# Kernel tuning notes

Hardware: AMD Instinct MI355X
Metric: run time of the kernel (lower is better)

Reference implementation:

```python
import jax, jax.numpy as jnp
import numpy as np

NUM_SYMBOLS = 5
NUM_SUBCARRIERS = 33


def _dft_matrix(n):
    # Unitary DFT matrix: F[j,k] = exp(-2i*pi*j*k/n) / sqrt(n)
    omega = np.exp(-2j * np.pi / n)
    j, k = np.meshgrid(np.arange(n), np.arange(n))
    return (np.power(omega, j * k) / np.sqrt(n)).astype(np.complex64)


def setup_inputs() -> dict:
    key = jax.random.key(0)
    k1, k2 = jax.random.split(key)
    shape = (4096, NUM_SYMBOLS, 4, 4, NUM_SUBCARRIERS)  # (N, S, TXH, TXW, W)
    x_real = jax.random.normal(k1, shape, dtype=jnp.float32)
    x_imag = jax.random.normal(k2, shape, dtype=jnp.float32)
    F_sym = _dft_matrix(NUM_SYMBOLS)
    F_sub = _dft_matrix(NUM_SUBCARRIERS)
    return {
        "x_real": x_real,
        "x_imag": x_imag,
        "F_sym_real": jnp.asarray(F_sym.real, dtype=jnp.float32),
        "F_sym_imag": jnp.asarray(F_sym.imag, dtype=jnp.float32),
        "F_sub_real": jnp.asarray(F_sub.real, dtype=jnp.float32),
        "F_sub_imag": jnp.asarray(F_sub.imag, dtype=jnp.float32),
    }


def reference(x_real, x_imag, F_sym_real, F_sym_imag, F_sub_real, F_sub_imag):
    N, S, TXH, TXW, W = x_real.shape
    x = jax.lax.complex(x_real, x_imag).reshape(N, S, TXH * TXW, W)
    x = jnp.transpose(x, (0, 2, 1, 3))  # (N, A, S, W), A = TXH*TXW

    F_sym = jax.lax.complex(F_sym_real, F_sym_imag)  # (S, S)
    F_sub = jax.lax.complex(F_sub_real, F_sub_imag)  # (W, W)

    # 2D DFT across symbols (left) and subcarriers (right)
    X = jnp.einsum("st,natw->nasw", F_sym, x)
    X = jnp.einsum("nasw,wv->nasv", X, F_sub)

    # magnitude-square (power spectrum)
    X_mag_sq = (X.real * X.real + X.imag * X.imag).astype(jnp.complex64)

    # inverse 2D DFT (conjugate transposes) -> autocorrelation
    X = jnp.einsum("st,natw->nasw", F_sym.conj().T, X_mag_sq)
    X = jnp.einsum("nasw,wv->nasv", X, F_sub.conj().T)

    X = jnp.transpose(X, (0, 2, 1, 3))  # (N, S, A, W)
    return X.reshape(N, S, TXH, TXW, W)
```

## Files before the change

### kernel.cpp

```cpp
#include <hip/hip_runtime.h>

#define NS 5
#define NW 33
#define NA 16
#define SW 165
#define BUFS 99
#define MPW 5
#define GM 20
#define TPM 11
#define CPT 3
#define THREADS 256

#define C0T 3
#define C0E (C0T*NW*MPW)
#define IT0 8
#define C1T 2
#define C1E (C1T*NW*MPW)
#define IT1 6

typedef float f2 __attribute__((ext_vector_type(2)));

__device__ __forceinline__ void cmac_re(f2& z, f2 u, f2 f) {
    asm("v_pk_fma_f32 %0, %1, %2, %0 op_sel:[0,0,0] op_sel_hi:[1,0,1]"
        : "+v"(z) : "v"(u), "v"(f));
}
__device__ __forceinline__ void cmac_im(f2& z, f2 d, f2 f) {
    asm("v_pk_fma_f32 %0, %1, %2, %0 op_sel:[1,1,0] op_sel_hi:[0,1,1] neg_lo:[1,0,0]"
        : "+v"(z) : "v"(d), "v"(f));
}
__device__ __forceinline__ void cmacr(f2& z, f2 f, f2 Pp) {
    asm("v_pk_fma_f32 %0, %1, %2, %0 op_sel:[0,0,0] op_sel_hi:[1,1,1] neg_hi:[1,0,0]"
        : "+v"(z) : "v"(f), "v"(Pp));
}
__device__ __forceinline__ void pkfma(f2& z, f2 a, f2 b) {
    asm("v_pk_fma_f32 %0, %1, %2, %0 op_sel:[0,0,0] op_sel_hi:[1,1,1]"
        : "+v"(z) : "v"(a), "v"(b));
}
__device__ __forceinline__ f2 pkadd(f2 a, f2 b) {
    f2 r; asm("v_pk_add_f32 %0, %1, %2" : "=v"(r) : "v"(a), "v"(b)); return r;
}
__device__ __forceinline__ f2 pksub(f2 a, f2 b) {
    f2 r; asm("v_pk_add_f32 %0, %1, %2 neg_lo:[0,1] neg_hi:[0,1]"
              : "=v"(r) : "v"(a), "v"(b)); return r;
}
__device__ __forceinline__ f2 pkaddsub(f2 a, f2 b) {
    f2 r; asm("v_pk_add_f32 %0, %1, %2 neg_hi:[0,1]"
              : "=v"(r) : "v"(a), "v"(b)); return r;
}
__device__ __forceinline__ f2 pkmul_re(f2 u, f2 f) {
    f2 r; asm("v_pk_mul_f32 %0, %1, %2 op_sel:[0,0] op_sel_hi:[1,0]"
              : "=v"(r) : "v"(u), "v"(f)); return r;
}
__device__ __forceinline__ f2 pkmul(f2 a, f2 b) {
    f2 r; asm("v_pk_mul_f32 %0, %1, %2" : "=v"(r) : "v"(a), "v"(b)); return r;
}

#define STAGE(NT, CE_, NIT, T0)                                            \
    {                                                                      \
        f2 rr[NIT]; int dsa[NIT];                                          \
        _Pragma("unroll")                                                  \
        for (int i = 0; i < NIT; ++i) {                                    \
            const int e = lane + i * 64;                                   \
            f2 v = (f2){0.f, 0.f};                                         \
            int da = 0;                                                    \
            if (e < (CE_)) {                                               \
                const int gq = e / ((NT) * NW), rq = e - gq * ((NT) * NW); \
                const int tq = rq / NW, wq = rq - tq * NW;                 \
                const int Mq = Mw + gq;                                    \
                da = gq * BUFS + wq * (NT) + tq;                           \
                if (Mq < NM) {                                             \
                    const int nq = Mq >> 4, aq = Mq & 15;                  \
                    const int go = (nq * NS + (T0) + tq) * (NA * NW) + aq * NW + wq; \
                    v = (f2){x_real[go], x_imag[go]};                      \
                }                                                          \
            }                                                              \
            rr[i] = v; dsa[i] = da;                                        \
        }                                                                  \
        _Pragma("unroll")                                                  \
        for (int i = 0; i < NIT; ++i) {                                    \
            const int e = lane + i * 64;                                   \
            if (e < (CE_)) wbuf[dsa[i]] = rr[i];                           \
        }                                                                  \
    }

#define COMPUTE_CHUNK(NT, TBASE)                                           \
    if (act) {                                                             \
        const f2* bp = wbuf + gg * BUFS;                                   \
        {                                               \
            f2 fv[CPT];                                                    \
            _Pragma("unroll")                                              \
            for (int k = 0; k < CPT; ++k) fv[k] = sFsub[c0 + k];           \
            _Pragma("unroll")                                              \
            for (int t = 0; t < (NT); ++t) {                               \
                const f2 xc = bp[t];                                       \
                _Pragma("unroll")                                          \
                for (int k = 0; k < CPT; ++k)                              \
                    V[(TBASE) + t][k] = pkmul_re(xc, fv[k]);               \
            }                                                              \
        }                                                                  \
        _Pragma("unroll 4")                                                \
        for (int wp = 1; wp <= 16; ++wp) {                                 \
            const int wq = NW - wp;                                        \
            f2 xcA[NT], xcB[NT];                                           \
            _Pragma("unroll")                                              \
            for (int t = 0; t < (NT); ++t) xcA[t] = bp[wp * (NT) + t];     \
            _Pragma("unroll")                                              \
            for (int t = 0; t < (NT); ++t) xcB[t] = bp[wq * (NT) + t];     \
            f2 fv[CPT];                                                    \
            _Pragma("unroll")                                              \
            for (int k = 0; k < CPT; ++k) fv[k] = sFsub[wp * NW + c0 + k]; \
            _Pragma("unroll")                                              \
            for (int t = 0; t < (NT); ++t) {                               \
                const f2 u = pkadd(xcA[t], xcB[t]);                        \
                const f2 d = pksub(xcA[t], xcB[t]);                        \
                _Pragma("unroll")                                          \
                for (int k = 0; k < CPT; ++k) {                            \
                    cmac_re(V[(TBASE) + t][k], u, fv[k]);                  \
                    cmac_im(V[(TBASE) + t][k], d, fv[k]);                  \
                }                                                          \
            }                                                              \
        }                                                                  \
    }

__global__ __launch_bounds__(THREADS, 6) void autocorr_kernel(
    const float* __restrict__ x_real, const float* __restrict__ x_imag,
    const float* __restrict__ Fsym_re, const float* __restrict__ Fsym_im,
    const float* __restrict__ Fsub_re, const float* __restrict__ Fsub_im,
    float* __restrict__ out, int NM, int write_complex)
{
    __shared__ f2 sFsym[NS * NS];
    __shared__ f2 sFsub[NW * NW];
    __shared__ f2 buf[GM * BUFS];

    const int tid = threadIdx.x;
    const int wave = tid >> 6;
    const int lane = tid & 63;
    const int Mw = blockIdx.x * GM + wave * MPW;
    f2* const wbuf = &buf[wave * MPW * BUFS];

    for (int i = tid; i < NW * NW; i += THREADS)
        sFsub[i] = (f2){Fsub_re[i], Fsub_im[i]};
    if (tid < NS * NS) sFsym[tid] = (f2){Fsym_re[tid], Fsym_im[tid]};

    STAGE(C0T, C0E, IT0, 0);
    __syncthreads();

    const int g = lane / TPM;
    const int j = lane - g * TPM;
    const bool act = (lane < MPW * TPM);
    const int gg = act ? g : 0;
    const int M = Mw + gg;
    const int c0 = 3 * j;

    f2 V[NS][CPT];

    COMPUTE_CHUNK(C0T, 0);

    STAGE(C1T, C1E, IT1, C0T);
    asm volatile("s_waitcnt lgkmcnt(0)" ::: "memory");

    COMPUTE_CHUNK(C1T, C0T);

    f2 T2[3][CPT];
#pragma unroll
    for (int p = 0; p < 3; ++p)
#pragma unroll
        for (int k = 0; k < CPT; ++k) T2[p][k] = (f2){0.f, 0.f};
    if (act) {
#pragma unroll
        for (int k = 0; k < CPT; ++k) {
            f2 a = V[1][k], b = V[4][k];
            V[1][k] = pkadd(a, b); V[4][k] = pksub(a, b);
            a = V[2][k]; b = V[3][k];
            V[2][k] = pkadd(a, b); V[3][k] = pksub(a, b);
        }
#pragma unroll
        for (int s = 0; s < NS; ++s) {
            const f2 f0 = sFsym[s * NS + 0];
            const f2 f1 = sFsym[s * NS + 1];
            const f2 fc2 = sFsym[s * NS + 2];
            f2 X[CPT];
#pragma unroll
            for (int k = 0; k < CPT; ++k) {
                X[k] = pkmul_re(V[0][k], f0);
                cmac_re(X[k], V[1][k], f1); cmac_im(X[k], V[4][k], f1);
                cmac_re(X[k], V[2][k], fc2); cmac_im(X[k], V[3][k], fc2);
            }
#pragma unroll
            for (int k = 0; k < CPT; ++k) {
                const float Pv = X[k].x * X[k].x + X[k].y * X[k].y;
                const f2 Pp = (f2){Pv, Pv};
#pragma unroll
                for (int p = 0; p < 3; ++p)
                    cmacr(T2[p][k], sFsym[s * NS + p], Pp);
            }
        }
        f2* const wb = wbuf + gg * BUFS;
#pragma unroll
        for (int k = 0; k < CPT; ++k)
#pragma unroll
            for (int p = 0; p < 3; ++p)
                wb[(c0 + k) * 3 + p] = T2[p][k];
    }
    asm volatile("s_waitcnt lgkmcnt(0)" ::: "memory");

    if (act) {
        const f2* bp = wbuf + gg * BUFS;
        if (!write_complex) {
            f2 Ypk[3][CPT];
            {
                f2 fw[CPT];
#pragma unroll
                for (int k = 0; k < CPT; ++k) fw[k] = sFsub[(c0 + k) * NW];
#pragma unroll
                for (int p = 0; p < 3; ++p) {
                    const f2 tc = bp[p];
#pragma unroll
                    for (int k = 0; k < CPT; ++k)
                        Ypk[p][k] = pkmul(tc, fw[k]);
                }
            }
#pragma unroll 4
            for (int vp = 1; vp <= 16; ++vp) {
                const int vq = NW - vp;
                f2 tcA[3], tcB[3];
#pragma unroll
                for (int p = 0; p < 3; ++p) tcA[p] = bp[vp * 3 + p];
#pragma unroll
                for (int p = 0; p < 3; ++p) tcB[p] = bp[vq * 3 + p];
                f2 e2[3];
#pragma unroll
                for (int p = 0; p < 3; ++p) e2[p] = pkaddsub(tcA[p], tcB[p]);
                f2 fw[CPT];
#pragma unroll
                for (int k = 0; k < CPT; ++k) fw[k] = sFsub[(c0 + k) * NW + vp];
#pragma unroll
                for (int p = 0; p < 3; ++p)
#pragma unroll
                    for (int k = 0; k < CPT; ++k)
                        pkfma(Ypk[p][k], e2[p], fw[k]);
            }
            if (M < NM) {
                const int n = M >> 4, a = M & 15;
                const int obase = ((n * NS) * NA + a) * NW;
#pragma unroll
                for (int p = 0; p < 3; ++p) {
                    const int pp = (NS - p) % NS;
#pragma unroll
                    for (int k = 0; k < CPT; ++k) {
                        const int q = c0 + k;
                        const int qq = (NW - q) % NW;
                        const float Yr = Ypk[p][k].x + Ypk[p][k].y;
                        out[obase + p * (NA * NW) + q] = Yr;
                        out[obase + pp * (NA * NW) + qq] = Yr;
                    }
                }
            }
        } else {
            f2 Y[3][CPT];
#pragma unroll
            for (int p = 0; p < 3; ++p)
#pragma unroll
                for (int k = 0; k < CPT; ++k) Y[p][k] = (f2){0.f, 0.f};
            for (int v = 0; v < NW; ++v) {
                f2 tc[3];
#pragma unroll
                for (int p = 0; p < 3; ++p) tc[p] = bp[v * 3 + p];
                f2 fw[CPT];
#pragma unroll
                for (int k = 0; k < CPT; ++k) fw[k] = sFsub[(c0 + k) * NW + v];
#pragma unroll
                for (int p = 0; p < 3; ++p)
#pragma unroll
                    for (int k = 0; k < CPT; ++k) {
                        Y[p][k].x = fmaf(tc[p].x, fw[k].x, Y[p][k].x);
                        Y[p][k].x = fmaf(tc[p].y, fw[k].y, Y[p][k].x);
                        Y[p][k].y = fmaf(tc[p].y, fw[k].x, Y[p][k].y);
                        Y[p][k].y = fmaf(-tc[p].x, fw[k].y, Y[p][k].y);
                    }
            }
            if (M < NM) {
                const int n = M >> 4, a = M & 15;
#pragma unroll
                for (int p = 0; p < 3; ++p) {
                    const int pp = (NS - p) % NS;
#pragma unroll
                    for (int k = 0; k < CPT; ++k) {
                        const int q = c0 + k;
                        const int qq = (NW - q) % NW;
                        ((float2*)out)[((n * NS + p) * NA + a) * NW + q] =
                            make_float2(Y[p][k].x, Y[p][k].y);
                        ((float2*)out)[((n * NS + pp) * NA + a) * NW + qq] =
                            make_float2(Y[p][k].x, -Y[p][k].y);
                    }
                }
            }
        }
    }
}

extern "C" void kernel_launch(void* const* d_in, const int* in_sizes, int n_in,
                              void* d_out, int out_size, void* d_ws, size_t ws_size,
                              hipStream_t stream) {
    const float* x_real  = (const float*)d_in[0];
    const float* x_imag  = (const float*)d_in[1];
    const float* Fsym_re = (const float*)d_in[2];
    const float* Fsym_im = (const float*)d_in[3];
    const float* Fsub_re = (const float*)d_in[4];
    const float* Fsub_im = (const float*)d_in[5];

    const int NM = in_sizes[0] / SW;
    const long long n_cplx = (long long)in_sizes[0];
    const int write_complex = ((long long)out_size >= 2 * n_cplx) ? 1 : 0;

    const int blocks = (NM + GM - 1) / GM;

    autocorr_kernel<<<blocks, THREADS, 0, stream>>>(
        x_real, x_imag, Fsym_re, Fsym_im, Fsub_re, Fsub_im,
        (float*)d_out, NM, write_complex);
}
```

Baseline: 175.6 us.

## Prefetch second input chunk into registers before first-chunk compute

Result: faster. 164.3 us (-6.4%).

```diff
diff --git a/kernel.cpp b/kernel.cpp
--- a/kernel.cpp
+++ b/kernel.cpp
@@ -55,32 +55,31 @@
     f2 r; asm("v_pk_mul_f32 %0, %1, %2" : "=v"(r) : "v"(a), "v"(b)); return r;
 }
 
-#define STAGE(NT, CE_, NIT, T0)                                            \
-    {                                                                      \
-        f2 rr[NIT]; int dsa[NIT];                                          \
-        _Pragma("unroll")                                                  \
-        for (int i = 0; i < NIT; ++i) {                                    \
-            const int e = lane + i * 64;                                   \
-            f2 v = (f2){0.f, 0.f};                                         \
-            int da = 0;                                                    \
-            if (e < (CE_)) {                                               \
-                const int gq = e / ((NT) * NW), rq = e - gq * ((NT) * NW); \
-                const int tq = rq / NW, wq = rq - tq * NW;                 \
-                const int Mq = Mw + gq;                                    \
-                da = gq * BUFS + wq * (NT) + tq;                           \
-                if (Mq < NM) {                                             \
-                    const int nq = Mq >> 4, aq = Mq & 15;                  \
-                    const int go = (nq * NS + (T0) + tq) * (NA * NW) + aq * NW + wq; \
-                    v = (f2){x_real[go], x_imag[go]};                      \
-                }                                                          \
+#define STAGE_LOAD(R, DS, NT, CE_, NIT, T0)                                \
+    _Pragma("unroll")                                                      \
+    for (int i = 0; i < NIT; ++i) {                                        \
+        const int e = lane + i * 64;                                       \
+        f2 v = (f2){0.f, 0.f};                                             \
+        int da = 0;                                                        \
+        if (e < (CE_)) {                                                   \
+            const int gq = e / ((NT) * NW), rq = e - gq * ((NT) * NW);     \
+            const int tq = rq / NW, wq = rq - tq * NW;                     \
+            const int Mq = Mw + gq;                                        \
+            da = gq * BUFS + wq * (NT) + tq;                               \
+            if (Mq < NM) {                                                 \
+                const int nq = Mq >> 4, aq = Mq & 15;                      \
+                const int go = (nq * NS + (T0) + tq) * (NA * NW) + aq * NW + wq; \
+                v = (f2){x_real[go], x_imag[go]};                          \
             }                                                              \
-            rr[i] = v; dsa[i] = da;                                        \
         }                                                                  \
-        _Pragma("unroll")                                                  \
-        for (int i = 0; i < NIT; ++i) {                                    \
-            const int e = lane + i * 64;                                   \
-            if (e < (CE_)) wbuf[dsa[i]] = rr[i];                           \
-        }                                                                  \
+        R[i] = v; DS[i] = da;                                              \
+    }
+
+#define STAGE_WRITE(R, DS, CE_, NIT)                                       \
+    _Pragma("unroll")                                                      \
+    for (int i = 0; i < NIT; ++i) {                                        \
+        const int e = lane + i * 64;                                       \
+        if (e < (CE_)) wbuf[DS[i]] = R[i];                                 \
     }
 
 #define COMPUTE_CHUNK(NT, TBASE)                                           \
@@ -122,7 +121,7 @@
         }                                                                  \
     }
 
-__global__ __launch_bounds__(THREADS, 6) void autocorr_kernel(
+__global__ __launch_bounds__(THREADS, 5) void autocorr_kernel(
     const float* __restrict__ x_real, const float* __restrict__ x_imag,
     const float* __restrict__ Fsym_re, const float* __restrict__ Fsym_im,
     const float* __restrict__ Fsub_re, const float* __restrict__ Fsub_im,
@@ -142,8 +141,15 @@
         sFsub[i] = (f2){Fsub_re[i], Fsub_im[i]};
     if (tid < NS * NS) sFsym[tid] = (f2){Fsym_re[tid], Fsym_im[tid]};
 
-    STAGE(C0T, C0E, IT0, 0);
+    {
+        f2 rr0[IT0]; int ds0[IT0];
+        STAGE_LOAD(rr0, ds0, C0T, C0E, IT0, 0);
+        STAGE_WRITE(rr0, ds0, C0E, IT0);
+    }
     __syncthreads();
+
+    f2 rr1[IT1]; int ds1[IT1];
+    STAGE_LOAD(rr1, ds1, C1T, C1E, IT1, C0T);
 
     const int g = lane / TPM;
     const int j = lane - g * TPM;
@@ -156,7 +162,7 @@
 
     COMPUTE_CHUNK(C0T, 0);
 
-    STAGE(C1T, C1E, IT1, C0T);
+    STAGE_WRITE(rr1, ds1, C1E, IT1);
     asm volatile("s_waitcnt lgkmcnt(0)" ::: "memory");
 
     COMPUTE_CHUNK(C1T, C0T);
@@ -223,14 +229,13 @@
 #pragma unroll 4
             for (int vp = 1; vp <= 16; ++vp) {
                 const int vq = NW - vp;
-                f2 tcA[3], tcB[3];
-#pragma unroll
-                for (int p = 0; p < 3; ++p) tcA[p] = bp[vp * 3 + p];
-#pragma unroll
-                for (int p = 0; p < 3; ++p) tcB[p] = bp[vq * 3 + p];
                 f2 e2[3];
 #pragma unroll
-                for (int p = 0; p < 3; ++p) e2[p] = pkaddsub(tcA[p], tcB[p]);
+                for (int p = 0; p < 3; ++p) {
+                    const f2 ta = bp[vp * 3 + p];
+                    const f2 tb = bp[vq * 3 + p];
+                    e2[p] = pkaddsub(ta, tb);
+                }
                 f2 fw[CPT];
 #pragma unroll
                 for (int k = 0; k < CPT; ++k) fw[k] = sFsub[(c0 + k) * NW + vp];
```
